# Optimization experiments

Hardware: AMD Instinct MI355X
Metric: run time of the kernel (lower is better)

The kernel has to match this reference:

```python
import jax, jax.numpy as jnp
import numpy as np

N = 100000
E = 3200000
IN_DIM = 256
HID = 128
OUT_DIM = 64


def setup_inputs() -> dict:
    key = jax.random.key(0)
    ks = jax.random.split(key, 8)
    features = jax.random.normal(ks[0], (N, IN_DIM), dtype=jnp.float32)
    edge_row = jax.random.randint(ks[1], (E,), 0, N, dtype=jnp.int32)
    edge_col = jax.random.randint(ks[2], (E,), 0, N, dtype=jnp.int32)
    edge_val = jax.random.uniform(ks[3], (E,), dtype=jnp.float32)
    W1 = jax.random.normal(ks[4], (IN_DIM, HID), dtype=jnp.float32) * (1.0 / np.sqrt(IN_DIM))
    b1 = jnp.zeros((HID,), dtype=jnp.float32)
    W2 = jax.random.normal(ks[5], (HID, OUT_DIM), dtype=jnp.float32) * (1.0 / np.sqrt(HID))
    b2 = jnp.zeros((OUT_DIM,), dtype=jnp.float32)
    return {"features": features, "edge_row": edge_row, "edge_col": edge_col,
            "edge_val": edge_val, "W1": W1, "b1": b1, "W2": W2, "b2": b2}


def reference(features, edge_row, edge_col, edge_val, W1, b1, W2, b2):
    # fc1: [N, IN_DIM] @ [IN_DIM, HID] + b1
    h = features @ W1 + b1                                   # [N, HID]
    # spmm(A, h): for each edge (r, c, v): out[r] += v * h[c]
    msgs = edge_val[:, None] * h[edge_col]                    # [E, HID] gather
    h = jax.ops.segment_sum(msgs, edge_row, num_segments=N)   # [N, HID] scatter-add
    h = jax.nn.relu(h)
    h = h @ W2 + b2                                           # [N, OUT_DIM]
    return jax.nn.log_softmax(h, axis=1)
```

## Files before the change

### kernel.cpp

```cpp
#include <hip/hip_runtime.h>
#include <math.h>

constexpr int IN_DIM  = 256;
constexpr int HID     = 128;
constexpr int OUT_DIM = 64;

constexpr int BROWS   = 128;
constexpr int NBUCK   = 782;
constexpr int CAP     = 4608;
constexpr int CHUNK   = 8192;

typedef short  bf16x8 __attribute__((ext_vector_type(8)));
typedef float  f32x4  __attribute__((ext_vector_type(4)));

__device__ __forceinline__ unsigned short f2bf(float x) {
    union { float f; unsigned u; } v; v.f = x;
    unsigned r = v.u + 0x7FFF + ((v.u >> 16) & 1);
    return (unsigned short)(r >> 16);
}

__global__ __launch_bounds__(256) void w1t_kernel(const float* __restrict__ W1,
                                                  unsigned short* __restrict__ W1T)
{
    int idx = blockIdx.x * 256 + threadIdx.x;
    int k = idx >> 7;
    int n = idx & 127;
    W1T[n * IN_DIM + k] = f2bf(W1[idx]);
}

constexpr int AROW = 36;

__global__ __launch_bounds__(256) void fc1_mfma(const float* __restrict__ feat,
                                                const unsigned short* __restrict__ W1T,
                                                const float* __restrict__ b1,
                                                unsigned short* __restrict__ h1b, int N)
{
    __shared__ unsigned short sA[64 * AROW];
    const int t    = threadIdx.x;
    const int lane = t & 63;
    const int w    = t >> 6;
    const int quad = lane >> 4;
    const int ln15 = lane & 15;
    const int row0 = blockIdx.x * 64;

    f32x4 acc[8];
#pragma unroll
    for (int i = 0; i < 8; ++i) acc[i] = (f32x4){0.f, 0.f, 0.f, 0.f};

    for (int ks = 0; ks < IN_DIM; ks += 32) {
#pragma unroll
        for (int i = 0; i < 2; ++i) {
            int idx = t + i * 256;
            int r   = idx >> 3;
            int k4  = idx & 7;
            int gr  = row0 + r;
            float4 v = make_float4(0.f, 0.f, 0.f, 0.f);
            if (gr < N)
                v = *(const float4*)&feat[(size_t)gr * IN_DIM + ks + k4 * 4];
            ushort4 o;
            o.x = f2bf(v.x); o.y = f2bf(v.y); o.z = f2bf(v.z); o.w = f2bf(v.w);
            *(ushort4*)&sA[r * AROW + k4 * 4] = o;
        }
        __syncthreads();

        bf16x8 afrag = *(const bf16x8*)&sA[(w * 16 + ln15) * AROW + quad * 8];
#pragma unroll
        for (int nt = 0; nt < 8; ++nt) {
            bf16x8 bfrag = *(const bf16x8*)&W1T[(size_t)(nt * 16 + ln15) * IN_DIM + ks + quad * 8];
            acc[nt] = __builtin_amdgcn_mfma_f32_16x16x32_bf16(afrag, bfrag, acc[nt], 0, 0, 0);
        }
        __syncthreads();
    }

#pragma unroll
    for (int nt = 0; nt < 8; ++nt) {
        int col = nt * 16 + ln15;
        float bias = b1[col];
#pragma unroll
        for (int r = 0; r < 4; ++r) {
            int grow = row0 + w * 16 + quad * 4 + r;
            if (grow < N)
                h1b[(size_t)grow * HID + col] = f2bf(acc[nt][r] + bias);
        }
    }
}

__global__ __launch_bounds__(256) void bin_kernel(const int* __restrict__ erow,
                                                  const int* __restrict__ ecol,
                                                  const float* __restrict__ eval,
                                                  int* __restrict__ gCursor,
                                                  int2* __restrict__ binned, int E)
{
    __shared__ int sCnt[NBUCK];
    __shared__ int sBase[NBUCK];
    const int t = threadIdx.x;
    const int e0 = blockIdx.x * CHUNK;
    const int eEnd = min(e0 + CHUNK, E);

    for (int i = t; i < NBUCK; i += 256) sCnt[i] = 0;
    __syncthreads();

    for (int e = e0 + t; e < eEnd; e += 256)
        atomicAdd(&sCnt[erow[e] >> 7], 1);
    __syncthreads();

    for (int i = t; i < NBUCK; i += 256) {
        int c = sCnt[i];
        sBase[i] = c ? atomicAdd(&gCursor[i], c) : 0;
        sCnt[i] = 0;
    }
    __syncthreads();

    for (int e = e0 + t; e < eEnd; e += 256) {
        int   r = erow[e];
        int   c = ecol[e];
        float v = eval[e];
        int   b = r >> 7;
        int off = sBase[b] + atomicAdd(&sCnt[b], 1);
        if (off < CAP)
            binned[(size_t)b * CAP + off] = make_int2(c | ((r & 127) << 17),
                                                      __float_as_int(v));
    }
}

__global__ __launch_bounds__(256) void sort_bucket(const int* __restrict__ gCursor,
                                                   const int2* __restrict__ binned,
                                                   int2* __restrict__ edges2,
                                                   int2* __restrict__ rowIdx, int N)
{
    __shared__ int2 sEdge[CAP];
    __shared__ unsigned short sOrd[CAP];
    __shared__ int sHist[BROWS];
    __shared__ int sStart[BROWS + 1];
    __shared__ int sCur[BROWS];
    const int t  = threadIdx.x;
    const int b  = blockIdx.x;
    const int nE = min(gCursor[b], CAP);
    const size_t base = (size_t)b * CAP;

    if (t < BROWS) sHist[t] = 0;
    __syncthreads();

    for (int i = t; i < nE; i += 256) {
        int2 p = binned[base + i];
        sEdge[i] = p;
        atomicAdd(&sHist[p.x >> 17], 1);
    }
    __syncthreads();

    if (t < BROWS) sStart[t + 1] = sHist[t];
    if (t == 0) sStart[0] = 0;
    __syncthreads();
    for (int o = 1; o < BROWS; o <<= 1) {
        int v = 0;
        if (t < BROWS) {
            v = sStart[t + 1];
            if (t >= o) v += sStart[t + 1 - o];
        }
        __syncthreads();
        if (t < BROWS) sStart[t + 1] = v;
        __syncthreads();
    }
    if (t < BROWS) sCur[t] = sStart[t];
    __syncthreads();

    for (int i = t; i < nE; i += 256) {
        int rl = sEdge[i].x >> 17;
        int pos = atomicAdd(&sCur[rl], 1);
        sOrd[pos] = (unsigned short)i;
    }
    __syncthreads();

    for (int i = t; i < nE; i += 256)
        edges2[base + i] = sEdge[sOrd[i]];

    if (t < BROWS) {
        int r = b * BROWS + t;
        if (r < N)
            rowIdx[r] = make_int2((int)base + sStart[t], (int)base + sStart[t + 1]);
    }
}

__device__ __forceinline__ void accum_row(const int2* __restrict__ edges2,
                                          const unsigned short* __restrict__ h1b,
                                          int j, int jend, int lane,
                                          float& ax, float& ay)
{
    ax = 0.f; ay = 0.f;
    for (; j + 3 < jend; j += 4) {
        int2 p0 = edges2[j];
        int2 p1 = edges2[j + 1];
        int2 p2 = edges2[j + 2];
        int2 p3 = edges2[j + 3];
        unsigned g0 = *(const unsigned*)&h1b[(size_t)(p0.x & 0x1FFFF) * HID + lane * 2];
        unsigned g1 = *(const unsigned*)&h1b[(size_t)(p1.x & 0x1FFFF) * HID + lane * 2];
        unsigned g2 = *(const unsigned*)&h1b[(size_t)(p2.x & 0x1FFFF) * HID + lane * 2];
        unsigned g3 = *(const unsigned*)&h1b[(size_t)(p3.x & 0x1FFFF) * HID + lane * 2];
        float v0 = __int_as_float(p0.y), v1 = __int_as_float(p1.y);
        float v2 = __int_as_float(p2.y), v3 = __int_as_float(p3.y);
        ax += v0 * __uint_as_float(g0 << 16); ay += v0 * __uint_as_float(g0 & 0xFFFF0000u);
        ax += v1 * __uint_as_float(g1 << 16); ay += v1 * __uint_as_float(g1 & 0xFFFF0000u);
        ax += v2 * __uint_as_float(g2 << 16); ay += v2 * __uint_as_float(g2 & 0xFFFF0000u);
        ax += v3 * __uint_as_float(g3 << 16); ay += v3 * __uint_as_float(g3 & 0xFFFF0000u);
    }
    for (; j < jend; ++j) {
        int2 p = edges2[j];
        unsigned g = *(const unsigned*)&h1b[(size_t)(p.x & 0x1FFFF) * HID + lane * 2];
        float v = __int_as_float(p.y);
        ax += v * __uint_as_float(g << 16);
        ay += v * __uint_as_float(g & 0xFFFF0000u);
    }
}

__global__ __launch_bounds__(256) void spmm_fc2_kernel(const int2* __restrict__ rowIdx,
                                                       const int2* __restrict__ edges2,
                                                       const unsigned short* __restrict__ h1b,
                                                       const float* __restrict__ W2,
                                                       const float* __restrict__ b2,
                                                       float* __restrict__ out, int N)
{
    const int lane = threadIdx.x & 63;
    const int wv   = (blockIdx.x * blockDim.x + threadIdx.x) >> 6;
    const int r0   = wv * 2;
    const int r1   = r0 + 1;
    if (r0 >= N) return;

    float ax0, ay0, ax1 = 0.f, ay1 = 0.f;
    int2 se0 = rowIdx[r0];
    accum_row(edges2, h1b, se0.x, se0.y, lane, ax0, ay0);
    if (r1 < N) {
        int2 se1 = rowIdx[r1];
        accum_row(edges2, h1b, se1.x, se1.y, lane, ax1, ay1);
    }

    ax0 = fmaxf(ax0, 0.f); ay0 = fmaxf(ay0, 0.f);
    ax1 = fmaxf(ax1, 0.f); ay1 = fmaxf(ay1, 0.f);

    float o0 = 0.f, o1 = 0.f;
#pragma unroll
    for (int j = 0; j < 64; ++j) {
        float w0 = W2[(2 * j) * OUT_DIM + lane];
        float w1 = W2[(2 * j + 1) * OUT_DIM + lane];
        o0 += __shfl(ax0, j) * w0 + __shfl(ay0, j) * w1;
        o1 += __shfl(ax1, j) * w0 + __shfl(ay1, j) * w1;
    }
    const float bias = b2[lane];
    o0 += bias; o1 += bias;

    float m0 = o0, m1 = o1;
#pragma unroll
    for (int o = 32; o > 0; o >>= 1) {
        m0 = fmaxf(m0, __shfl_xor(m0, o));
        m1 = fmaxf(m1, __shfl_xor(m1, o));
    }
    float s0 = __expf(o0 - m0), s1 = __expf(o1 - m1);
#pragma unroll
    for (int o = 32; o > 0; o >>= 1) {
        s0 += __shfl_xor(s0, o);
        s1 += __shfl_xor(s1, o);
    }
    out[(size_t)r0 * OUT_DIM + lane] = o0 - m0 - __logf(s0);
    if (r1 < N)
        out[(size_t)r1 * OUT_DIM + lane] = o1 - m1 - __logf(s1);
}

extern "C" void kernel_launch(void* const* d_in, const int* in_sizes, int n_in,
                              void* d_out, int out_size, void* d_ws, size_t ws_size,
                              hipStream_t stream) {
    const float* feat = (const float*)d_in[0];
    const int*   erow = (const int*)d_in[1];
    const int*   ecol = (const int*)d_in[2];
    const float* eval = (const float*)d_in[3];
    const float* W1   = (const float*)d_in[4];
    const float* b1   = (const float*)d_in[5];
    const float* W2   = (const float*)d_in[6];
    const float* b2   = (const float*)d_in[7];
    float*       out  = (float*)d_out;

    const int N = in_sizes[0] / IN_DIM;
    const int E = in_sizes[1];

    unsigned short* h1b    = (unsigned short*)d_ws;
    int2*           binned = (int2*)(h1b + (size_t)N * HID);
    int2*           edges2 = binned + (size_t)NBUCK * CAP;
    int2*           rowIdx = edges2 + (size_t)NBUCK * CAP;
    unsigned short* W1T    = (unsigned short*)(rowIdx + N);
    int*            gCursor= (int*)(W1T + IN_DIM * HID);

    hipMemsetAsync(gCursor, 0, NBUCK * sizeof(int), stream);

    w1t_kernel<<<(IN_DIM * HID) / 256, 256, 0, stream>>>(W1, W1T);
    fc1_mfma<<<(N + 63) / 64, 256, 0, stream>>>(feat, W1T, b1, h1b, N);
    bin_kernel<<<(E + CHUNK - 1) / CHUNK, 256, 0, stream>>>(erow, ecol, eval,
                                                            gCursor, binned, E);
    sort_bucket<<<NBUCK, 256, 0, stream>>>(gCursor, binned, edges2, rowIdx, N);

    const int nwaves = (N + 1) / 2;
    const int nblk   = (nwaves + 3) / 4;
    spmm_fc2_kernel<<<nblk, 256, 0, stream>>>(rowIdx, edges2, h1b, W2, b2, out, N);
}
```

Measured before the change: 512.2 us.

## Preload full feature tile in fc1, pre-scale edge column offsets, unroll gather by 8

fc1 now converts and stores the whole 64x256 feature tile to shared memory once, then runs all eight MFMA k-steps without per-step barriers. The binning stage stores the column index pre-shifted into a byte offset (c<<8, i.e. c*256 bytes per bf16 row), with the local row moved into the top 7 bits. The SpMM gather then takes a direct byte-address add instead of a multiply, and its loop is unrolled to 8 edges to keep more loads in flight. The larger shared tile (about 33KB) may lower fc1 occupancy, and the packed field relies on c*256 fitting in 25 bits.

```diff
diff --git a/kernel.cpp b/kernel.cpp
--- a/kernel.cpp
+++ b/kernel.cpp
@@ -28,14 +28,14 @@
     W1T[n * IN_DIM + k] = f2bf(W1[idx]);
 }
 
-constexpr int AROW = 36;
+constexpr int PADK = 264;
 
 __global__ __launch_bounds__(256) void fc1_mfma(const float* __restrict__ feat,
                                                 const unsigned short* __restrict__ W1T,
                                                 const float* __restrict__ b1,
                                                 unsigned short* __restrict__ h1b, int N)
 {
-    __shared__ unsigned short sA[64 * AROW];
+    __shared__ unsigned short sA[64 * PADK];
     const int t    = threadIdx.x;
     const int lane = t & 63;
     const int w    = t >> 6;
@@ -43,33 +43,33 @@
     const int ln15 = lane & 15;
     const int row0 = blockIdx.x * 64;
 
+#pragma unroll
+    for (int i = 0; i < 16; ++i) {
+        int flat = i * 256 + t;
+        int r    = flat >> 6;
+        int k4   = flat & 63;
+        int gr   = row0 + r;
+        float4 v = make_float4(0.f, 0.f, 0.f, 0.f);
+        if (gr < N)
+            v = *(const float4*)&feat[(size_t)gr * IN_DIM + k4 * 4];
+        ushort4 o;
+        o.x = f2bf(v.x); o.y = f2bf(v.y); o.z = f2bf(v.z); o.w = f2bf(v.w);
+        *(ushort4*)&sA[r * PADK + k4 * 4] = o;
+    }
+    __syncthreads();
+
     f32x4 acc[8];
 #pragma unroll
     for (int i = 0; i < 8; ++i) acc[i] = (f32x4){0.f, 0.f, 0.f, 0.f};
 
-    for (int ks = 0; ks < IN_DIM; ks += 32) {
-#pragma unroll
-        for (int i = 0; i < 2; ++i) {
-            int idx = t + i * 256;
-            int r   = idx >> 3;
-            int k4  = idx & 7;
-            int gr  = row0 + r;
-            float4 v = make_float4(0.f, 0.f, 0.f, 0.f);
-            if (gr < N)
-                v = *(const float4*)&feat[(size_t)gr * IN_DIM + ks + k4 * 4];
-            ushort4 o;
-            o.x = f2bf(v.x); o.y = f2bf(v.y); o.z = f2bf(v.z); o.w = f2bf(v.w);
-            *(ushort4*)&sA[r * AROW + k4 * 4] = o;
-        }
-        __syncthreads();
-
-        bf16x8 afrag = *(const bf16x8*)&sA[(w * 16 + ln15) * AROW + quad * 8];
+#pragma unroll
+    for (int ks = 0; ks < 8; ++ks) {
+        bf16x8 afrag = *(const bf16x8*)&sA[(w * 16 + ln15) * PADK + ks * 32 + quad * 8];
 #pragma unroll
         for (int nt = 0; nt < 8; ++nt) {
-            bf16x8 bfrag = *(const bf16x8*)&W1T[(size_t)(nt * 16 + ln15) * IN_DIM + ks + quad * 8];
+            bf16x8 bfrag = *(const bf16x8*)&W1T[(size_t)(nt * 16 + ln15) * IN_DIM + ks * 32 + quad * 8];
             acc[nt] = __builtin_amdgcn_mfma_f32_16x16x32_bf16(afrag, bfrag, acc[nt], 0, 0, 0);
         }
-        __syncthreads();
     }
 
 #pragma unroll
@@ -118,7 +118,7 @@
         int   b = r >> 7;
         int off = sBase[b] + atomicAdd(&sCnt[b], 1);
         if (off < CAP)
-            binned[(size_t)b * CAP + off] = make_int2(c | ((r & 127) << 17),
+            binned[(size_t)b * CAP + off] = make_int2((c << 8) | ((r & 127) << 25),
                                                       __float_as_int(v));
     }
 }
@@ -144,7 +144,7 @@
     for (int i = t; i < nE; i += 256) {
         int2 p = binned[base + i];
         sEdge[i] = p;
-        atomicAdd(&sHist[p.x >> 17], 1);
+        atomicAdd(&sHist[(unsigned)p.x >> 25], 1);
     }
     __syncthreads();
 
@@ -165,7 +165,7 @@
     __syncthreads();
 
     for (int i = t; i < nE; i += 256) {
-        int rl = sEdge[i].x >> 17;
+        int rl = (unsigned)sEdge[i].x >> 25;
         int pos = atomicAdd(&sCur[rl], 1);
         sOrd[pos] = (unsigned short)i;
     }
@@ -182,30 +182,29 @@
 }
 
 __device__ __forceinline__ void accum_row(const int2* __restrict__ edges2,
-                                          const unsigned short* __restrict__ h1b,
-                                          int j, int jend, int lane,
+                                          const char* __restrict__ h1base,
+                                          int j, int jend, int lane4,
                                           float& ax, float& ay)
 {
     ax = 0.f; ay = 0.f;
-    for (; j + 3 < jend; j += 4) {
-        int2 p0 = edges2[j];
-        int2 p1 = edges2[j + 1];
-        int2 p2 = edges2[j + 2];
-        int2 p3 = edges2[j + 3];
-        unsigned g0 = *(const unsigned*)&h1b[(size_t)(p0.x & 0x1FFFF) * HID + lane * 2];
-        unsigned g1 = *(const unsigned*)&h1b[(size_t)(p1.x & 0x1FFFF) * HID + lane * 2];
-        unsigned g2 = *(const unsigned*)&h1b[(size_t)(p2.x & 0x1FFFF) * HID + lane * 2];
-        unsigned g3 = *(const unsigned*)&h1b[(size_t)(p3.x & 0x1FFFF) * HID + lane * 2];
-        float v0 = __int_as_float(p0.y), v1 = __int_as_float(p1.y);
-        float v2 = __int_as_float(p2.y), v3 = __int_as_float(p3.y);
-        ax += v0 * __uint_as_float(g0 << 16); ay += v0 * __uint_as_float(g0 & 0xFFFF0000u);
-        ax += v1 * __uint_as_float(g1 << 16); ay += v1 * __uint_as_float(g1 & 0xFFFF0000u);
-        ax += v2 * __uint_as_float(g2 << 16); ay += v2 * __uint_as_float(g2 & 0xFFFF0000u);
-        ax += v3 * __uint_as_float(g3 << 16); ay += v3 * __uint_as_float(g3 & 0xFFFF0000u);
+    for (; j + 7 < jend; j += 8) {
+        int2 p[8];
+#pragma unroll
+        for (int u = 0; u < 8; ++u) p[u] = edges2[j + u];
+        unsigned g[8];
+#pragma unroll
+        for (int u = 0; u < 8; ++u)
+            g[u] = *(const unsigned*)(h1base + ((p[u].x & 0x01FFFFFF) + lane4));
+#pragma unroll
+        for (int u = 0; u < 8; ++u) {
+            float v = __int_as_float(p[u].y);
+            ax += v * __uint_as_float(g[u] << 16);
+            ay += v * __uint_as_float(g[u] & 0xFFFF0000u);
+        }
     }
     for (; j < jend; ++j) {
         int2 p = edges2[j];
-        unsigned g = *(const unsigned*)&h1b[(size_t)(p.x & 0x1FFFF) * HID + lane * 2];
+        unsigned g = *(const unsigned*)(h1base + ((p.x & 0x01FFFFFF) + lane4));
         float v = __int_as_float(p.y);
         ax += v * __uint_as_float(g << 16);
         ay += v * __uint_as_float(g & 0xFFFF0000u);
@@ -219,18 +218,20 @@
                                                        const float* __restrict__ b2,
                                                        float* __restrict__ out, int N)
 {
-    const int lane = threadIdx.x & 63;
-    const int wv   = (blockIdx.x * blockDim.x + threadIdx.x) >> 6;
-    const int r0   = wv * 2;
-    const int r1   = r0 + 1;
+    const int lane  = threadIdx.x & 63;
+    const int lane4 = lane * 4;
+    const int wv    = (blockIdx.x * blockDim.x + threadIdx.x) >> 6;
+    const int r0    = wv * 2;
+    const int r1    = r0 + 1;
     if (r0 >= N) return;
+    const char* h1base = (const char*)h1b;
 
     float ax0, ay0, ax1 = 0.f, ay1 = 0.f;
     int2 se0 = rowIdx[r0];
-    accum_row(edges2, h1b, se0.x, se0.y, lane, ax0, ay0);
+    accum_row(edges2, h1base, se0.x, se0.y, lane4, ax0, ay0);
     if (r1 < N) {
         int2 se1 = rowIdx[r1];
-        accum_row(edges2, h1b, se1.x, se1.y, lane, ax1, ay1);
+        accum_row(edges2, h1base, se1.x, se1.y, lane4, ax1, ay1);
     }
 
     ax0 = fmaxf(ax0, 0.f); ay0 = fmaxf(ay0, 0.f);
```

New measurement: 525.0 us. 1.02x slower.
